# Optimization experiments

Hardware: AMD Instinct MI355X
Metric: run time of the kernel (lower is better)

## Reference

```python
import jax, jax.numpy as jnp
import numpy as np

B, S, V = 2048, 200, 50257
E, H, EMB = 60, 30, 20  # encode_size, hidden_size, embed_size


def setup_inputs() -> dict:
    key = jax.random.key(0)
    ks = jax.random.split(key, 24)
    emb = jax.random.normal(ks[7], (V, EMB), jnp.float32) * 0.02
    emb = emb.at[3].set(0.0)  # padding_idx=3
    inp = {
        'coverage': jax.random.uniform(ks[0], (B, S), jnp.float32),
        'enc_out': jax.random.normal(ks[1], (B, S, E), jnp.float32),
        'h0': jax.random.normal(ks[2], (1, B, H), jnp.float32),
        'c0': jax.random.normal(ks[3], (1, B, H), jnp.float32),
        'attn': jax.random.uniform(ks[4], (B, S), jnp.float32),
        'dec_input': jax.random.randint(ks[5], (B, 1), 0, V, jnp.int32),
        'enc_inputs': jax.random.randint(ks[6], (B, S), 0, V, jnp.int32),
        'embedding': emb,
        # LSTM (torch gate order i,f,g,o)
        'w_ih': jax.random.normal(ks[8], (4 * H, EMB + E), jnp.float32) * 0.1,
        'w_hh': jax.random.normal(ks[9], (4 * H, H), jnp.float32) * 0.1,
        'b_ih': jax.random.normal(ks[10], (4 * H,), jnp.float32) * 0.1,
        'b_hh': jax.random.normal(ks[11], (4 * H,), jnp.float32) * 0.1,
        # Attention submodule
        'attn_wh_w': jax.random.normal(ks[12], (H, E), jnp.float32) * 0.1,
        'attn_wh_b': jax.random.normal(ks[13], (H,), jnp.float32) * 0.1,
        'attn_ws_w': jax.random.normal(ks[14], (H, H), jnp.float32) * 0.1,
        'attn_ws_b': jax.random.normal(ks[15], (H,), jnp.float32) * 0.1,
        'attn_wc': jax.random.uniform(ks[16], (H,), jnp.float32),
        'attn_v': jax.random.uniform(ks[17], (H,), jnp.float32),
        # pointer-gen params
        'wh': jax.random.uniform(ks[18], (E,), jnp.float32),
        'ws': jax.random.uniform(ks[19], (H,), jnp.float32),
        'wx': jax.random.uniform(ks[20], (EMB,), jnp.float32),
        'v_w': jax.random.normal(ks[21], (V, H), jnp.float32) * 0.02,
        'v_b': jax.random.normal(ks[22], (V,), jnp.float32) * 0.02,
    }
    return inp


def reference(coverage, enc_out, h0, c0, attn, dec_input, enc_inputs, embedding,
              w_ih, w_hh, b_ih, b_hh, attn_wh_w, attn_wh_b, attn_ws_w, attn_ws_b,
              attn_wc, attn_v, wh, ws, wx, v_w, v_b):
    # context = bmm(attn[B,1,S], enc_out[B,S,E]) -> [B,E]
    context = jnp.einsum('bs,bse->be', attn, enc_out)
    embed = embedding[dec_input[:, 0]]              # [B,EMB]
    x = jnp.concatenate([context, embed], axis=-1)  # [B,E+EMB]
    # single-step LSTM (torch gate order i,f,g,o)
    gates = x @ w_ih.T + b_ih + h0[0] @ w_hh.T + b_hh
    i, f, g, o = jnp.split(gates, 4, axis=-1)
    c = jax.nn.sigmoid(f) * c0[0] + jax.nn.sigmoid(i) * jnp.tanh(g)
    h = jax.nn.sigmoid(o) * jnp.tanh(c)             # rnn_out [B,H]
    p_vocab = jax.nn.softmax(h @ v_w.T + v_b, axis=1)   # [B,V]
    p_gen = jax.nn.sigmoid(context @ wh + h @ ws + embed @ wx)[:, None]  # [B,1]
    # attention
    wh_app = enc_out @ attn_wh_w.T + attn_wh_b      # [B,S,H]
    ws_app = (h @ attn_ws_w.T + attn_ws_b)[:, None, :]  # [B,1,H]
    wc_app = coverage[..., None] * attn_wc          # [B,S,H]
    energy = jnp.tanh(wh_app + ws_app + wc_app) @ attn_v  # [B,S]
    new_attn = jax.nn.softmax(energy, axis=1)
    coverage_loss = jnp.sum(jnp.minimum(new_attn, coverage))
    new_coverage = coverage + new_attn
    # scatter copy-attention into vocab space (duplicate idx: arbitrary winner, as torch scatter_)
    rows = jnp.arange(enc_inputs.shape[0])[:, None]
    attn_scores = jnp.zeros((enc_inputs.shape[0], v_w.shape[0]), p_vocab.dtype).at[rows, enc_inputs].set(new_attn)
    output = p_gen * p_vocab + (1.0 - p_gen) * attn_scores
    return output, new_coverage, (h[None], c[None]), new_attn, coverage_loss
```

## Files before the change

kernel.cpp:

```cpp
#include <hip/hip_runtime.h>

#define BB 2048
#define SS 200
#define VV 50257
#define EE 60
#define HH 30
#define EMBD 20
#define XD 80
#define G4 120
#define NCHUNK 50
#define VPAD 51200
#define SROW 68

#define O_COV ((size_t)BB*VV)
#define O_H   (O_COV + (size_t)BB*SS)
#define O_C   (O_H + (size_t)BB*HH)
#define O_NA  (O_C + (size_t)BB*HH)
#define O_LOSS (O_NA + (size_t)BB*SS)

typedef __attribute__((ext_vector_type(8))) short short8v;
typedef __attribute__((ext_vector_type(4))) float f32x4;

__device__ __forceinline__ float sigf(float x){ return 1.f/(1.f+__expf(-x)); }

__device__ __forceinline__ short f2bf(float f){
  union { __bf16 h; short s; } u; u.h = (__bf16)f; return u.s;
}

__device__ __forceinline__ float bsum(float v, float* red, int tid){
  #pragma unroll
  for (int off=32; off; off>>=1) v += __shfl_xor(v, off);
  __syncthreads();
  if ((tid&63)==0) red[tid>>6]=v;
  __syncthreads();
  return red[0]+red[1]+red[2]+red[3];
}
__device__ __forceinline__ float bmax(float v, float* red, int tid){
  #pragma unroll
  for (int off=32; off; off>>=1) v = fmaxf(v, __shfl_xor(v, off));
  __syncthreads();
  if ((tid&63)==0) red[tid>>6]=v;
  __syncthreads();
  return fmaxf(fmaxf(red[0],red[1]),fmaxf(red[2],red[3]));
}

__global__ __launch_bounds__(256) void k_pack(
  const float* __restrict__ v_w, const float* __restrict__ v_b,
  short* __restrict__ vw_bf, float* __restrict__ vb_pad)
{
  const int idx = blockIdx.x*256 + threadIdx.x;
  const int col = idx>>2, q = idx&3;
  union { short8v v; short s[8]; } u;
  #pragma unroll
  for (int j=0;j<8;j++){
    int k = q*8+j;
    u.s[j] = (col<VV && k<HH) ? f2bf(v_w[(size_t)col*HH+k]) : (short)0;
  }
  ((short8v*)vw_bf)[idx] = u.v;
  if (q==0) vb_pad[col] = (col<VV) ? v_b[col] : -1e30f;
}

__global__ __launch_bounds__(256) void k_row(
  const float* __restrict__ coverage, const float* __restrict__ enc_out,
  const float* __restrict__ h0, const float* __restrict__ c0,
  const float* __restrict__ attn, const int* __restrict__ dec_input,
  const float* __restrict__ embedding,
  const float* __restrict__ w_ih, const float* __restrict__ w_hh,
  const float* __restrict__ b_ih, const float* __restrict__ b_hh,
  const float* __restrict__ attn_wh_w, const float* __restrict__ attn_wh_b,
  const float* __restrict__ attn_ws_w, const float* __restrict__ attn_ws_b,
  const float* __restrict__ attn_wc, const float* __restrict__ attn_v,
  const float* __restrict__ whv, const float* __restrict__ wsv, const float* __restrict__ wxv,
  float* __restrict__ out, float* __restrict__ pgen_ws,
  float* __restrict__ losspart_ws, short* __restrict__ h_bf)
{
  const int b = blockIdx.x, tid = threadIdx.x;
  __shared__ float enc[SS*61];
  __shared__ float wT[EE*32];
  __shared__ float attn_s[SS], cov_s[SS];
  __shared__ float xls[XD], hls[HH], wsapp[HH], wc_s[HH], v_s[HH], gls[G4];
  __shared__ float ctxp[EE*4];
  __shared__ float red[4];

  {
    const float4* ep = (const float4*)(enc_out + (size_t)b*(SS*EE));
    #pragma unroll
    for (int it=0; it<12; ++it){
      int i = tid + it*256;
      if (i < (SS*EE/4)) {
        float4 v = ep[i];
        int s = i/15, e4 = (i - s*15)*4;
        float* d = &enc[s*61+e4];
        d[0]=v.x; d[1]=v.y; d[2]=v.z; d[3]=v.w;
      }
    }
  }
  if (tid < SS) { attn_s[tid]=attn[(size_t)b*SS+tid]; cov_s[tid]=coverage[(size_t)b*SS+tid]; }
  for (int i=tid; i<EE*HH; i+=256){ int h=i/EE, e=i-h*EE; wT[e*32+h]=attn_wh_w[i]; }
  if (tid >= 256-HH) { int h = tid-(256-HH); wc_s[h]=attn_wc[h]; v_s[h]=attn_v[h]; }
  __syncthreads();

  if (tid < 240){
    int g = tid/60, e = tid - g*60;
    float acc=0.f;
    for (int s=g; s<SS; s+=4) acc += attn_s[s]*enc[s*61+e];
    ctxp[e*4+g]=acc;
  }
  __syncthreads();
  if (tid < EE) xls[tid]=ctxp[tid*4]+ctxp[tid*4+1]+ctxp[tid*4+2]+ctxp[tid*4+3];
  else if (tid < EE+EMBD){
    int k = tid-EE;
    int dix = dec_input[b];
    xls[tid] = embedding[(size_t)dix*EMBD+k];
  }
  __syncthreads();

  if (tid < G4){
    float acc = b_ih[tid]+b_hh[tid];
    const float* wi = w_ih + tid*XD;
    #pragma unroll
    for (int k=0;k<XD;k++) acc += xls[k]*wi[k];
    const float* whh = w_hh + tid*HH;
    const float* h0b = h0 + (size_t)b*HH;
    #pragma unroll
    for (int k=0;k<HH;k++) acc += h0b[k]*whh[k];
    gls[tid]=acc;
  }
  __syncthreads();
  if (tid < HH){
    float c = sigf(gls[tid+HH])*c0[(size_t)b*HH+tid] + sigf(gls[tid])*tanhf(gls[tid+2*HH]);
    float h = sigf(gls[tid+3*HH])*tanhf(c);
    out[O_C+(size_t)b*HH+tid]=c;
    out[O_H+(size_t)b*HH+tid]=h;
    hls[tid]=h;
  }
  __syncthreads();
  if (tid < 4){
    union { short8v v; short s[8]; } u;
    #pragma unroll
    for (int j=0;j<8;j++){ int k=tid*8+j; u.s[j] = (k<HH)? f2bf(hls[k]) : (short)0; }
    ((short8v*)(h_bf + (size_t)b*32))[tid] = u.v;
  }
  if (tid < HH){
    float acc = attn_ws_b[tid] + attn_wh_b[tid];
    const float* w = attn_ws_w + tid*HH;
    #pragma unroll
    for (int k=0;k<HH;k++) acc += hls[k]*w[k];
    wsapp[tid]=acc;
  }
  float pv=0.f;
  if (tid<EE) pv = xls[tid]*whv[tid];
  else if (tid<EE+HH) pv = hls[tid-EE]*wsv[tid-EE];
  else if (tid<EE+HH+EMBD) pv = xls[EE+(tid-EE-HH)]*wxv[tid-EE-HH];
  float pg = sigf(bsum(pv,red,tid));
  if (tid==0) pgen_ws[b]=pg;
  __syncthreads();

  float en = -1e30f;
  if (tid < SS){
    float acc[HH];
    float cv = cov_s[tid];
    #pragma unroll
    for (int h=0;h<HH;h++) acc[h] = wsapp[h] + cv*wc_s[h];
    for (int e=0;e<EE;e++){
      float evv = enc[tid*61+e];
      #pragma unroll
      for (int h=0;h<HH;h++) acc[h] += evv*wT[e*32+h];
    }
    float e2=0.f;
    #pragma unroll
    for (int h=0;h<HH;h++) e2 += tanhf(acc[h])*v_s[h];
    en = e2;
  }
  float mx = bmax(en, red, tid);
  float ex = (tid<SS)? __expf(en-mx) : 0.f;
  float sm = bsum(ex, red, tid);
  float inv = 1.f/sm;
  float lossv = 0.f;
  if (tid<SS){
    float na = ex*inv;
    float cv = cov_s[tid];
    out[O_NA+(size_t)b*SS+tid]=na;
    out[O_COV+(size_t)b*SS+tid]=cv+na;
    lossv = fminf(na,cv);
  }
  float ls = bsum(lossv,red,tid);
  if (tid==0) losspart_ws[b]=ls;
}

__global__ __launch_bounds__(256) void k_vsum(
  const short* __restrict__ vw_bf, const float* __restrict__ vb_pad,
  const short* __restrict__ h_bf, float* __restrict__ partial)
{
  const int tid = threadIdx.x;
  const int w = tid>>6, l = tid&63;
  const int lc = l&15, lg = l>>4;
  const int task = blockIdx.x*4 + w;
  const int rg = task & 127, cg = task >> 7;
  const int rbase = rg*16, cbase = cg*1024;

  short8v Af = *(const short8v*)(h_bf + (size_t)(rbase+lc)*32 + lg*8);

  float psum[4] = {0.f,0.f,0.f,0.f};
  #pragma unroll 4
  for (int t=0;t<64;t++){
    const int col = cbase + t*16 + lc;
    short8v Bf = *(const short8v*)(vw_bf + (size_t)col*32 + lg*8);
    const float vb = vb_pad[col];
    f32x4 z = {0.f,0.f,0.f,0.f};
    f32x4 d = __builtin_amdgcn_mfma_f32_16x16x32_bf16(Af, Bf, z, 0,0,0);
    psum[0] += __expf(d[0]+vb);
    psum[1] += __expf(d[1]+vb);
    psum[2] += __expf(d[2]+vb);
    psum[3] += __expf(d[3]+vb);
  }
  #pragma unroll
  for (int r=0;r<4;r++){
    float s = psum[r];
    s += __shfl_xor(s,1); s += __shfl_xor(s,2); s += __shfl_xor(s,4); s += __shfl_xor(s,8);
    if (lc==0) partial[(size_t)cg*BB + rbase + lg*4 + r] = s;
  }
}

__global__ __launch_bounds__(256) void k_off(
  const float* __restrict__ partial, const float* __restrict__ pgen,
  float* __restrict__ offs)
{
  const int row = blockIdx.x*256 + threadIdx.x;
  float s=0.f;
  #pragma unroll 5
  for (int c=0;c<NCHUNK;c++) s += partial[(size_t)c*BB + row];
  offs[row] = __logf(pgen[row]) - __logf(s);
}

__global__ __launch_bounds__(256) void k_vwrite(
  const short* __restrict__ vw_bf, const float* __restrict__ vb_pad,
  const short* __restrict__ h_bf, const float* __restrict__ offs,
  float* __restrict__ out)
{
  __shared__ short h_lds[16*32];
  __shared__ float stage[4][16*SROW];
  const int tid = threadIdx.x;
  const int rbase = blockIdx.x*16;
  const int cbase = blockIdx.y*2048;
  if (tid < 64) ((uint4*)h_lds)[tid] = ((const uint4*)(h_bf + (size_t)rbase*32))[tid];
  __syncthreads();

  const int w = tid>>6, l = tid&63;
  const int lc = l&15, lg = l>>4;

  short8v Af = *(const short8v*)&h_lds[lc*32 + lg*8];
  float offv[4];
  #pragma unroll
  for (int r=0;r<4;r++) offv[r] = offs[rbase + lg*4 + r];

  float* sw = stage[w];
  const int wc0 = cbase + w*512;

  for (int c=0;c<8;c++){
    const int c0 = wc0 + c*64;
    #pragma unroll
    for (int t=0;t<4;t++){
      const int col = c0 + t*16 + lc;
      short8v Bf = *(const short8v*)(vw_bf + (size_t)col*32 + lg*8);
      const float vb = vb_pad[col];
      f32x4 z = {0.f,0.f,0.f,0.f};
      f32x4 d = __builtin_amdgcn_mfma_f32_16x16x32_bf16(Af, Bf, z, 0,0,0);
      #pragma unroll
      for (int r=0;r<4;r++)
        sw[(lg*4+r)*SROW + t*16 + lc] = __expf(d[r]+vb+offv[r]);
    }
    #pragma unroll 4
    for (int i=0;i<16;i++){
      if (c0 + l < VV)
        out[(size_t)(rbase+i)*VV + c0 + l] = sw[i*SROW + l];
    }
  }
}

__global__ __launch_bounds__(256) void k_scatter(
  const int* __restrict__ enc_inputs, const float* __restrict__ pgen,
  const float* __restrict__ na, float* __restrict__ out)
{
  __shared__ int idx_s[SS];
  const int b=blockIdx.x, tid=threadIdx.x;
  if (tid<SS) idx_s[tid]=enc_inputs[(size_t)b*SS+tid];
  __syncthreads();
  if (tid<SS){
    int idx=idx_s[tid];
    bool last=true;
    for (int s2=tid+1;s2<SS;s2++) if (idx_s[s2]==idx){ last=false; break; }
    if (last){
      float add=(1.f-pgen[b])*na[(size_t)b*SS+tid];
      out[(size_t)b*VV+idx]+=add;
    }
  }
}

__global__ __launch_bounds__(256) void k_loss(const float* __restrict__ lp, float* __restrict__ dst){
  __shared__ float red[4];
  int tid=threadIdx.x;
  float s=0.f;
  for (int i=tid;i<BB;i+=256) s+=lp[i];
  #pragma unroll
  for (int off=32; off; off>>=1) s+=__shfl_xor(s,off);
  if ((tid&63)==0) red[tid>>6]=s;
  __syncthreads();
  if (tid==0) dst[0]=red[0]+red[1]+red[2]+red[3];
}

extern "C" void kernel_launch(void* const* d_in, const int* in_sizes, int n_in,
                              void* d_out, int out_size, void* d_ws, size_t ws_size,
                              hipStream_t stream)
{
  const float* coverage =(const float*)d_in[0];
  const float* enc_out  =(const float*)d_in[1];
  const float* h0       =(const float*)d_in[2];
  const float* c0       =(const float*)d_in[3];
  const float* attn     =(const float*)d_in[4];
  const int*   dec_input=(const int*)d_in[5];
  const int*   enc_inputs=(const int*)d_in[6];
  const float* embedding=(const float*)d_in[7];
  const float* w_ih     =(const float*)d_in[8];
  const float* w_hh     =(const float*)d_in[9];
  const float* b_ih     =(const float*)d_in[10];
  const float* b_hh     =(const float*)d_in[11];
  const float* attn_wh_w=(const float*)d_in[12];
  const float* attn_wh_b=(const float*)d_in[13];
  const float* attn_ws_w=(const float*)d_in[14];
  const float* attn_ws_b=(const float*)d_in[15];
  const float* attn_wc  =(const float*)d_in[16];
  const float* attn_v   =(const float*)d_in[17];
  const float* whv      =(const float*)d_in[18];
  const float* wsv      =(const float*)d_in[19];
  const float* wxv      =(const float*)d_in[20];
  const float* v_w      =(const float*)d_in[21];
  const float* v_b      =(const float*)d_in[22];
  float* out=(float*)d_out;
  float* wsf=(float*)d_ws;
  float* pgen    = wsf;
  float* losspart= wsf + 2048;
  float* offs    = wsf + 4096;
  float* partial = wsf + 6144;
  float* vb_pad  = wsf + 6144 + (size_t)NCHUNK*BB;
  short* vw_bf   = (short*)(vb_pad + VPAD);
  short* h_bf    = vw_bf + (size_t)VPAD*32;

  k_pack<<<VPAD*4/256,256,0,stream>>>(v_w,v_b,vw_bf,vb_pad);

  k_row<<<BB,256,0,stream>>>(coverage,enc_out,h0,c0,attn,dec_input,embedding,
    w_ih,w_hh,b_ih,b_hh,attn_wh_w,attn_wh_b,attn_ws_w,attn_ws_b,attn_wc,attn_v,
    whv,wsv,wxv,out,pgen,losspart,h_bf);

  k_vsum  <<<1600,256,0,stream>>>(vw_bf,vb_pad,h_bf,partial);
  k_off   <<<BB/256,256,0,stream>>>(partial,pgen,offs);
  dim3 gw(BB/16, VPAD/2048);
  k_vwrite<<<gw,256,0,stream>>>(vw_bf,vb_pad,h_bf,offs,out);
  k_scatter<<<BB,256,0,stream>>>(enc_inputs,pgen,out+O_NA,out);
  k_loss<<<1,256,0,stream>>>(losspart,out+O_LOSS);
}
```

Measured before the change: 332.6 us.

## Widen vocab logit staging tile and write output with aligned nontemporal vector stores

```diff
diff --git a/kernel.cpp b/kernel.cpp
--- a/kernel.cpp
+++ b/kernel.cpp
@@ -10,7 +10,7 @@
 #define G4 120
 #define NCHUNK 50
 #define VPAD 51200
-#define SROW 68
+#define SROW 132
 
 #define O_COV ((size_t)BB*VV)
 #define O_H   (O_COV + (size_t)BB*SS)
@@ -257,10 +257,10 @@
   float* sw = stage[w];
   const int wc0 = cbase + w*512;
 
-  for (int c=0;c<8;c++){
-    const int c0 = wc0 + c*64;
-    #pragma unroll
-    for (int t=0;t<4;t++){
+  for (int c=0;c<4;c++){
+    const int c0 = wc0 + c*128;
+    #pragma unroll
+    for (int t=0;t<8;t++){
       const int col = c0 + t*16 + lc;
       short8v Bf = *(const short8v*)(vw_bf + (size_t)col*32 + lg*8);
       const float vb = vb_pad[col];
@@ -270,10 +270,37 @@
       for (int r=0;r<4;r++)
         sw[(lg*4+r)*SROW + t*16 + lc] = __expf(d[r]+vb+offv[r]);
     }
-    #pragma unroll 4
-    for (int i=0;i<16;i++){
-      if (c0 + l < VV)
-        out[(size_t)(rbase+i)*VV + c0 + l] = sw[i*SROW + l];
+    if (c0 + 128 <= VV){
+      #pragma unroll 2
+      for (int i=0;i<16;i++){
+        const size_t g = (size_t)(rbase+i)*VV + c0;
+        const int p = (int)((4u - ((unsigned)g & 3u)) & 3u);
+        const float* sp = &sw[i*SROW];
+        if (l < 32){
+          const int K = p ? 31 : 32;
+          if (l < K){
+            const int o = p + l*4;
+            f32x4 vv = { sp[o], sp[o+1], sp[o+2], sp[o+3] };
+            __builtin_nontemporal_store(vv, (f32x4*)(out + g + o));
+          }
+        } else if (l < 32+p){
+          const int o = l - 32;
+          __builtin_nontemporal_store(sp[o], out + g + o);
+        } else if (p && l >= 40 && l < 40 + (4-p)){
+          const int o = p + 124 + (l - 40);
+          __builtin_nontemporal_store(sp[o], out + g + o);
+        }
+      }
+    } else {
+      for (int i=0;i<16;i++){
+        const size_t g = (size_t)(rbase+i)*VV;
+        #pragma unroll
+        for (int j=0;j<2;j++){
+          const int ci = c0 + j*64 + l;
+          if (ci < VV)
+            __builtin_nontemporal_store(sw[i*SROW + (ci - c0)], out + g + ci);
+        }
+      }
     }
   }
 }
```

Measured after the change: 384.1 us. +15.5%, slower.

## Fuse copy-attention scatter into vocab write kernel with shared-memory staging

Applied to the files above, without the earlier changes.

```diff
diff --git a/kernel.cpp b/kernel.cpp
--- a/kernel.cpp
+++ b/kernel.cpp
@@ -10,7 +10,7 @@
 #define G4 120
 #define NCHUNK 50
 #define VPAD 51200
-#define SROW 68
+#define CROW 524
 
 #define O_COV ((size_t)BB*VV)
 #define O_H   (O_COV + (size_t)BB*SS)
@@ -236,14 +236,38 @@
 __global__ __launch_bounds__(256) void k_vwrite(
   const short* __restrict__ vw_bf, const float* __restrict__ vb_pad,
   const short* __restrict__ h_bf, const float* __restrict__ offs,
-  float* __restrict__ out)
+  const float* __restrict__ pgen, const int* __restrict__ enc_inputs,
+  const float* __restrict__ na_src, float* __restrict__ out)
 {
   __shared__ short h_lds[16*32];
-  __shared__ float stage[4][16*SROW];
+  __shared__ float stage[16*CROW];
   const int tid = threadIdx.x;
   const int rbase = blockIdx.x*16;
-  const int cbase = blockIdx.y*2048;
+  const int cstart = blockIdx.y*12800;
   if (tid < 64) ((uint4*)h_lds)[tid] = ((const uint4*)(h_bf + (size_t)rbase*32))[tid];
+
+  int* sidx = (int*)stage;
+  for (int e=tid; e<16*SS; e+=256){
+    int i = e/SS, s = e - i*SS;
+    sidx[e] = enc_inputs[(size_t)(rbase+i)*SS + s];
+  }
+  __syncthreads();
+  int   ridx[13]; float rval[13]; int rrow[13];
+  #pragma unroll
+  for (int k=0;k<13;k++){
+    const int e = tid + k*256;
+    ridx[k] = -1; rrow[k] = 0; rval[k] = 0.f;
+    if (e < 16*SS){
+      const int i = e/SS, s = e - i*SS;
+      const int idx = sidx[e];
+      bool last = true;
+      for (int s2=s+1; s2<SS; s2++) if (sidx[i*SS+s2]==idx){ last=false; break; }
+      if (last){
+        ridx[k] = idx; rrow[k] = i;
+        rval[k] = (1.f - pgen[rbase+i]) * na_src[(size_t)(rbase+i)*SS + s];
+      }
+    }
+  }
   __syncthreads();
 
   const int w = tid>>6, l = tid&63;
@@ -254,46 +278,36 @@
   #pragma unroll
   for (int r=0;r<4;r++) offv[r] = offs[rbase + lg*4 + r];
 
-  float* sw = stage[w];
-  const int wc0 = cbase + w*512;
-
-  for (int c=0;c<8;c++){
-    const int c0 = wc0 + c*64;
-    #pragma unroll
-    for (int t=0;t<4;t++){
-      const int col = c0 + t*16 + lc;
+  for (int c=0;c<25;c++){
+    const int c0 = cstart + c*512;
+    #pragma unroll
+    for (int t=0;t<8;t++){
+      const int cl = w*128 + t*16 + lc;
+      const int col = c0 + cl;
       short8v Bf = *(const short8v*)(vw_bf + (size_t)col*32 + lg*8);
       const float vb = vb_pad[col];
       f32x4 z = {0.f,0.f,0.f,0.f};
       f32x4 d = __builtin_amdgcn_mfma_f32_16x16x32_bf16(Af, Bf, z, 0,0,0);
       #pragma unroll
       for (int r=0;r<4;r++)
-        sw[(lg*4+r)*SROW + t*16 + lc] = __expf(d[r]+vb+offv[r]);
-    }
-    #pragma unroll 4
+        stage[(lg*4+r)*CROW + cl] = __expf(d[r]+vb+offv[r]);
+    }
+    __syncthreads();
+    #pragma unroll
+    for (int k=0;k<13;k++){
+      if ((unsigned)(ridx[k]-c0) < 512u)
+        stage[rrow[k]*CROW + (ridx[k]-c0)] += rval[k];
+    }
+    __syncthreads();
     for (int i=0;i<16;i++){
-      if (c0 + l < VV)
-        out[(size_t)(rbase+i)*VV + c0 + l] = sw[i*SROW + l];
-    }
-  }
-}
-
-__global__ __launch_bounds__(256) void k_scatter(
-  const int* __restrict__ enc_inputs, const float* __restrict__ pgen,
-  const float* __restrict__ na, float* __restrict__ out)
-{
-  __shared__ int idx_s[SS];
-  const int b=blockIdx.x, tid=threadIdx.x;
-  if (tid<SS) idx_s[tid]=enc_inputs[(size_t)b*SS+tid];
-  __syncthreads();
-  if (tid<SS){
-    int idx=idx_s[tid];
-    bool last=true;
-    for (int s2=tid+1;s2<SS;s2++) if (idx_s[s2]==idx){ last=false; break; }
-    if (last){
-      float add=(1.f-pgen[b])*na[(size_t)b*SS+tid];
-      out[(size_t)b*VV+idx]+=add;
-    }
+      const size_t g = (size_t)(rbase+i)*VV;
+      #pragma unroll
+      for (int j=0;j<2;j++){
+        const int col = c0 + j*256 + tid;
+        if (col < VV) out[g + col] = stage[i*CROW + j*256 + tid];
+      }
+    }
+    __syncthreads();
   }
 }
 
@@ -354,8 +368,7 @@
 
   k_vsum  <<<1600,256,0,stream>>>(vw_bf,vb_pad,h_bf,partial);
   k_off   <<<BB/256,256,0,stream>>>(partial,pgen,offs);
-  dim3 gw(BB/16, VPAD/2048);
-  k_vwrite<<<gw,256,0,stream>>>(vw_bf,vb_pad,h_bf,offs,out);
-  k_scatter<<<BB,256,0,stream>>>(enc_inputs,pgen,out+O_NA,out);
+  dim3 gw(BB/16, 4);
+  k_vwrite<<<gw,256,0,stream>>>(vw_bf,vb_pad,h_bf,offs,pgen,enc_inputs,out+O_NA,out);
   k_loss<<<1,256,0,stream>>>(losspart,out+O_LOSS);
 }
```

After: 456.2 us. 37.2% more time.
